# Kernel optimization log

Measured on AMD Instinct MI355X. Metric: run time of the kernel, lower is better.

## Reference

```python
import jax, jax.numpy as jnp
import numpy as np

B, C, H, W = 32, 256, 32, 32
C8 = C // 8


def setup_inputs() -> dict:
    key = jax.random.key(0)
    ks = jax.random.split(key, 8)
    s = 1.0 / np.sqrt(C)
    return {
        "x": jax.random.normal(ks[0], (B, C, H, W), dtype=jnp.float32),
        "Wq": jax.random.normal(ks[1], (C8, C), dtype=jnp.float32) * s,
        "bq": jax.random.normal(ks[2], (C8,), dtype=jnp.float32) * s,
        "Wk": jax.random.normal(ks[3], (C8, C), dtype=jnp.float32) * s,
        "bk": jax.random.normal(ks[4], (C8,), dtype=jnp.float32) * s,
        "Wv": jax.random.normal(ks[5], (C, C), dtype=jnp.float32) * s,
        "bv": jax.random.normal(ks[6], (C,), dtype=jnp.float32) * s,
        "gamma": jax.random.normal(ks[7], (1,), dtype=jnp.float32) * 0.1,
    }


def reference(x, Wq, bq, Wk, bk, Wv, bv, gamma):
    b, c, h, w = x.shape
    n = h * w
    xf = x.reshape(b, c, n)  # [B, C, N]
    # 1x1 convs == per-pixel linear projections
    q = jnp.einsum('dc,bcn->bnd', Wq, xf) + bq            # [B, N, C/8]
    k = jnp.einsum('dc,bcn->bdn', Wk, xf) + bk[:, None]    # [B, C/8, N]
    v = jnp.einsum('dc,bcn->bdn', Wv, xf) + bv[:, None]    # [B, C, N]
    energy = jnp.einsum('bnd,bdm->bnm', q, k)              # [B, N, N], no scaling (as in source)
    attn = jax.nn.softmax(energy, axis=-1)                 # softmax over keys
    # out[:, :, i] = sum_j V[:, :, j] * attn[i, j]
    out = jnp.einsum('bdn,bmn->bdm', v, attn)              # [B, C, N]
    out = out.reshape(b, c, h, w)
    return gamma * out + x
```

## Files before the change

### kernel.cpp

```cpp
#include <hip/hip_runtime.h>
#include <math.h>

#define BB 32
#define CC 256
#define CQ 32
#define NN 1024

typedef short bf16x8 __attribute__((ext_vector_type(8)));
typedef float f32x4  __attribute__((ext_vector_type(4)));
typedef unsigned short u16;

__device__ __forceinline__ u16 f2bf(float f) {
    unsigned u = __float_as_uint(f);
    u = (u + 0x7FFFu + ((u >> 16) & 1u)) >> 16;
    return (u16)u;
}

__device__ __forceinline__ unsigned cvt_pk_bf16(float lo, float hi) {
    unsigned r;
    asm("v_cvt_pk_bf16_f32 %0, %1, %2" : "=v"(r) : "v"(lo), "v"(hi));
    return r;
}

__global__ void wpack_kernel(const float* __restrict__ Wq,
                             const float* __restrict__ Wk,
                             const float* __restrict__ Wv,
                             u16* __restrict__ wfrag)
{
    const int o = blockIdx.x * 256 + threadIdx.x;
    const int j    = o & 7;
    const int lane = (o >> 3) & 63;
    const int kc   = (o >> 9) & 7;
    const int rt   = o >> 12;
    const int row  = rt * 16 + (lane & 15);
    const int col  = kc * 32 + (lane >> 4) * 8 + j;
    const float v = (row < 32) ? Wq[row * 256 + col]
                  : (row < 64) ? Wk[(row - 32) * 256 + col]
                               : Wv[(row - 64) * 256 + col];
    wfrag[o] = f2bf(v);
}

struct QSmem {
    union {
        u16 xs[64][268];
        u16 osv[CC][72];
    };
    u16 osqk[64][72];
};

__global__ __launch_bounds__(256, 2) void qkv_kernel(
    const float* __restrict__ x, const u16* __restrict__ wfrag,
    const float* __restrict__ bq, const float* __restrict__ bk,
    const float* __restrict__ bv,
    u16* __restrict__ qt, u16* __restrict__ kt, u16* __restrict__ vv)
{
    __shared__ QSmem sm;
    const int b = blockIdx.y, n0 = blockIdx.x * 64;
    const int t = threadIdx.x;
    const int lane = t & 63, w = t >> 6;
    const int quad = lane >> 4, c16 = lane & 15;

    {
        const float* xb = x + (size_t)b * CC * NN + n0;
        const int n2 = 2 * (lane & 31);
        const int cr = w * 2 + (lane >> 5);
        float2 f[32];
#pragma unroll
        for (int it = 0; it < 32; ++it)
            f[it] = *(const float2*)(xb + (size_t)(it * 8 + cr) * NN + n2);
#pragma unroll
        for (int it = 0; it < 32; ++it) {
            const int c = it * 8 + cr;
            sm.xs[n2 + 0][c] = f2bf(f[it].x);
            sm.xs[n2 + 1][c] = f2bf(f[it].y);
        }
    }
    __syncthreads();

    f32x4 acc[5][4];
#pragma unroll
    for (int i = 0; i < 5; ++i)
#pragma unroll
        for (int j = 0; j < 4; ++j) acc[i][j] = (f32x4){0.f, 0.f, 0.f, 0.f};

#pragma unroll 2
    for (int k = 0; k < 8; ++k) {
        const int c0 = k * 32;
        bf16x8 wa[5], xb[4];
#pragma unroll
        for (int rs = 0; rs < 5; ++rs)
            wa[rs] = *(const bf16x8*)&wfrag[(size_t)(((w * 5 + rs) * 8 + k) * 64 + lane) * 8];
#pragma unroll
        for (int ns = 0; ns < 4; ++ns) {
            const short4 a = *(const short4*)&sm.xs[ns * 16 + c16][c0 + quad * 8];
            const short4 b2 = *(const short4*)&sm.xs[ns * 16 + c16][c0 + quad * 8 + 4];
            bf16x8 v;
            v[0] = a.x; v[1] = a.y; v[2] = a.z; v[3] = a.w;
            v[4] = b2.x; v[5] = b2.y; v[6] = b2.z; v[7] = b2.w;
            xb[ns] = v;
        }
#pragma unroll
        for (int rs = 0; rs < 5; ++rs)
#pragma unroll
            for (int ns = 0; ns < 4; ++ns)
                acc[rs][ns] = __builtin_amdgcn_mfma_f32_16x16x32_bf16(
                    wa[rs], xb[ns], acc[rs][ns], 0, 0, 0);
    }

    __syncthreads();

#pragma unroll
    for (int rs = 0; rs < 5; ++rs) {
#pragma unroll
        for (int r = 0; r < 4; ++r) {
            const int rg = w * 80 + rs * 16 + quad * 4 + r;
            const float bias = (rg < 32) ? bq[rg] : (rg < 64) ? bk[rg - 32] : bv[rg - 64];
#pragma unroll
            for (int ns = 0; ns < 4; ++ns) {
                const int n = ns * 16 + c16;
                const u16 h = f2bf(acc[rs][ns][r] + bias);
                if (rg < 64) sm.osqk[n][rg] = h;
                else         sm.osv[rg - 64][n] = h;
            }
        }
    }
    __syncthreads();

    {
        u16* dst = (w >= 2) ? kt : qt;
        const int dof = (w >= 2) ? 32 : 0;
        const int wl = w & 1;
        const size_t base = ((size_t)b * NN + n0) * CQ;
#pragma unroll
        for (int it = 0; it < 4; ++it) {
            const int o = wl * 2048 + it * 512 + lane * 8;
            const int n = o >> 5, d = o & 31;
            const bf16x8 v = *(const bf16x8*)&sm.osqk[n][d + dof];
            *(bf16x8*)&dst[base + o] = v;
        }
    }
#pragma unroll
    for (int it = 0; it < 8; ++it) {
        const int o = it * 2048 + t * 8;
        const int c = o >> 6, n = o & 63;
        const bf16x8 v = *(const bf16x8*)&sm.osv[c][n];
        *(bf16x8*)&vv[((size_t)b * CC + c) * NN + n0 + n] = v;
    }
}

__global__ __launch_bounds__(512, 4) void attn_kernel(
    const u16* __restrict__ qt, const u16* __restrict__ kt,
    const u16* __restrict__ vv, const float* __restrict__ x,
    const float* __restrict__ gamma_p, float* __restrict__ out)
{
    __shared__ u16 ps16[2][64][72];
    __shared__ float lsh[64];

    const int bid  = blockIdx.x;
    const int xcd  = bid & 7;
    const int slot = bid >> 3;
    const int b    = (xcd << 2) | (slot >> 4);
    const int m0   = (slot & 15) * 64;

    const int t = threadIdx.x, lane = t & 63, w = t >> 6;
    const int quad = lane >> 4, c16 = lane & 15;
    const int ch   = c16 >> 3;
    const int c7   = c16 & 7;
    const int qkey = (c16 >> 2) & 3;
    const int sm   = w & 3;
    const int sh   = w >> 2;
    const int ms0  = w & 3;

    const bf16x8 qa = *(const bf16x8*)&qt[((size_t)b * NN + m0 + sm * 16 + c16) * CQ + quad * 8];

    bf16x8 ones;
#pragma unroll
    for (int j = 0; j < 8; ++j) ones[j] = (short)0x3F80;

    f32x4 accO[2][4];
    f32x4 lsum = (f32x4){0.f, 0.f, 0.f, 0.f};
#pragma unroll
    for (int cs = 0; cs < 2; ++cs)
#pragma unroll
        for (int j = 0; j < 4; ++j) accO[cs][j] = (f32x4){0.f, 0.f, 0.f, 0.f};

    const u16* vbase = vv + (size_t)b * CC * NN;
    const u16* kbase = kt + (size_t)b * NN * CQ;

    bf16x8 kb[2];
#pragma unroll
    for (int s = 0; s < 2; ++s)
        kb[s] = *(const bf16x8*)&kbase[(size_t)(sh * 32 + s * 16 + c16) * CQ + quad * 8];

    for (int step = 0; step < 16; ++step) {
        const int nbase = step * 64;
        u16* psb = &ps16[step & 1][0][0];

        bf16x8 va[2][2];
#pragma unroll
        for (int cs = 0; cs < 2; ++cs)
#pragma unroll
            for (int kc = 0; kc < 2; ++kc)
                va[cs][kc] = *(const bf16x8*)&vbase[
                    (size_t)(w * 32 + cs * 16 + c16) * NN + nbase + kc * 32 + quad * 8];

        f32x4 accS[2];
#pragma unroll
        for (int s = 0; s < 2; ++s)
            accS[s] = __builtin_amdgcn_mfma_f32_16x16x32_bf16(
                qa, kb[s], (f32x4){0.f, 0.f, 0.f, 0.f}, 0, 0, 0);

        const int rowb = sm * 16 + quad * 4;
#pragma unroll
        for (int s = 0; s < 2; ++s) {
            const int nb = (sh * 4 + 2 * s + ch) ^ quad;
            u16* pw = &psb[rowb * 72 + nb * 8 + c7];
            const float e0 = __expf(accS[s][0]);
            const float e1 = __expf(accS[s][1]);
            const float e2 = __expf(accS[s][2]);
            const float e3 = __expf(accS[s][3]);
            const unsigned p01 = cvt_pk_bf16(e0, e1);
            const unsigned p23 = cvt_pk_bf16(e2, e3);
            pw[0]       = (u16)p01;
            pw[72]      = (u16)(p01 >> 16);
            pw[144]     = (u16)p23;
            pw[216]     = (u16)(p23 >> 16);
        }

        if (step < 15) {
#pragma unroll
            for (int s = 0; s < 2; ++s)
                kb[s] = *(const bf16x8*)&kbase[
                    (size_t)(nbase + 64 + sh * 32 + s * 16 + c16) * CQ + quad * 8];
        }

        __syncthreads();

#pragma unroll
        for (int msi = 0; msi < 4; ++msi) {
            bf16x8 pb[2];
#pragma unroll
            for (int kc = 0; kc < 2; ++kc)
                pb[kc] = *(const bf16x8*)&psb[(msi * 16 + c16) * 72
                                              + (4 * kc + (quad ^ qkey)) * 8];
            if (msi == ms0) {
                lsum = __builtin_amdgcn_mfma_f32_16x16x32_bf16(ones, pb[0], lsum, 0, 0, 0);
                lsum = __builtin_amdgcn_mfma_f32_16x16x32_bf16(ones, pb[1], lsum, 0, 0, 0);
            }
#pragma unroll
            for (int cs = 0; cs < 2; ++cs)
#pragma unroll
                for (int kc = 0; kc < 2; ++kc)
                    accO[cs][msi] = __builtin_amdgcn_mfma_f32_16x16x32_bf16(
                        va[cs][kc], pb[kc], accO[cs][msi], 0, 0, 0);
        }
    }

    if (sh == 0 && quad == 0) lsh[ms0 * 16 + c16] = lsum[0];
    __syncthreads();

    const float gamma = gamma_p[0];
#pragma unroll
    for (int ms = 0; ms < 4; ++ms) {
        const float inv = gamma / lsh[ms * 16 + c16];
        const int m = m0 + ms * 16 + c16;
#pragma unroll
        for (int cs = 0; cs < 2; ++cs) {
            const int cbase = w * 32 + cs * 16 + quad * 4;
#pragma unroll
            for (int r = 0; r < 4; ++r) {
                const size_t idx = ((size_t)b * CC + cbase + r) * NN + m;
                out[idx] = accO[cs][ms][r] * inv + x[idx];
            }
        }
    }
}

extern "C" void kernel_launch(void* const* d_in, const int* in_sizes, int n_in,
                              void* d_out, int out_size, void* d_ws, size_t ws_size,
                              hipStream_t stream)
{
    const float* x  = (const float*)d_in[0];
    const float* Wq = (const float*)d_in[1];
    const float* bq = (const float*)d_in[2];
    const float* Wk = (const float*)d_in[3];
    const float* bk = (const float*)d_in[4];
    const float* Wv = (const float*)d_in[5];
    const float* bv = (const float*)d_in[6];
    const float* gm = (const float*)d_in[7];
    float* out = (float*)d_out;

    u16* qt    = (u16*)d_ws;
    u16* kt    = qt + (size_t)BB * NN * CQ;
    u16* vv    = kt + (size_t)BB * NN * CQ;
    u16* wfrag = vv + (size_t)BB * CC * NN;

    wpack_kernel<<<320, 256, 0, stream>>>(Wq, Wk, Wv, wfrag);
    dim3 grid(16, BB);
    qkv_kernel<<<grid, 256, 0, stream>>>(x, wfrag, bq, bk, bv, qt, kt, vv);
    attn_kernel<<<512, 512, 0, stream>>>(qt, kt, vv, x, gm, out);
}
```

Baseline: 152.9 us.

## Halve QKV pixel tile and double attention key-step width with priority hints

```diff
diff --git a/kernel.cpp b/kernel.cpp
--- a/kernel.cpp
+++ b/kernel.cpp
@@ -42,56 +42,58 @@
 
 struct QSmem {
     union {
-        u16 xs[64][268];
-        u16 osv[CC][72];
+        u16 xs[32][268];
+        u16 osv[CC][40];
     };
-    u16 osqk[64][72];
+    u16 osqk[32][72];
 };
 
-__global__ __launch_bounds__(256, 2) void qkv_kernel(
+__global__ __launch_bounds__(256, 4) void qkv_kernel(
     const float* __restrict__ x, const u16* __restrict__ wfrag,
     const float* __restrict__ bq, const float* __restrict__ bk,
     const float* __restrict__ bv,
     u16* __restrict__ qt, u16* __restrict__ kt, u16* __restrict__ vv)
 {
     __shared__ QSmem sm;
-    const int b = blockIdx.y, n0 = blockIdx.x * 64;
+    const int b = blockIdx.y, n0 = blockIdx.x * 32;
     const int t = threadIdx.x;
     const int lane = t & 63, w = t >> 6;
     const int quad = lane >> 4, c16 = lane & 15;
 
     {
         const float* xb = x + (size_t)b * CC * NN + n0;
-        const int n2 = 2 * (lane & 31);
-        const int cr = w * 2 + (lane >> 5);
-        float2 f[32];
-#pragma unroll
-        for (int it = 0; it < 32; ++it)
-            f[it] = *(const float2*)(xb + (size_t)(it * 8 + cr) * NN + n2);
-#pragma unroll
-        for (int it = 0; it < 32; ++it) {
-            const int c = it * 8 + cr;
-            sm.xs[n2 + 0][c] = f2bf(f[it].x);
-            sm.xs[n2 + 1][c] = f2bf(f[it].y);
+        const int n4 = (t & 7) * 4;
+        const int cr = t >> 3;
+        float4 f[8];
+#pragma unroll
+        for (int it = 0; it < 8; ++it)
+            f[it] = *(const float4*)(xb + (size_t)(it * 32 + cr) * NN + n4);
+#pragma unroll
+        for (int it = 0; it < 8; ++it) {
+            const int c = it * 32 + cr;
+            sm.xs[n4 + 0][c] = f2bf(f[it].x);
+            sm.xs[n4 + 1][c] = f2bf(f[it].y);
+            sm.xs[n4 + 2][c] = f2bf(f[it].z);
+            sm.xs[n4 + 3][c] = f2bf(f[it].w);
         }
     }
     __syncthreads();
 
-    f32x4 acc[5][4];
+    f32x4 acc[5][2];
 #pragma unroll
     for (int i = 0; i < 5; ++i)
 #pragma unroll
-        for (int j = 0; j < 4; ++j) acc[i][j] = (f32x4){0.f, 0.f, 0.f, 0.f};
+        for (int j = 0; j < 2; ++j) acc[i][j] = (f32x4){0.f, 0.f, 0.f, 0.f};
 
 #pragma unroll 2
     for (int k = 0; k < 8; ++k) {
         const int c0 = k * 32;
-        bf16x8 wa[5], xb[4];
+        bf16x8 wa[5], xb[2];
 #pragma unroll
         for (int rs = 0; rs < 5; ++rs)
             wa[rs] = *(const bf16x8*)&wfrag[(size_t)(((w * 5 + rs) * 8 + k) * 64 + lane) * 8];
 #pragma unroll
-        for (int ns = 0; ns < 4; ++ns) {
+        for (int ns = 0; ns < 2; ++ns) {
             const short4 a = *(const short4*)&sm.xs[ns * 16 + c16][c0 + quad * 8];
             const short4 b2 = *(const short4*)&sm.xs[ns * 16 + c16][c0 + quad * 8 + 4];
             bf16x8 v;
@@ -102,7 +104,7 @@
 #pragma unroll
         for (int rs = 0; rs < 5; ++rs)
 #pragma unroll
-            for (int ns = 0; ns < 4; ++ns)
+            for (int ns = 0; ns < 2; ++ns)
                 acc[rs][ns] = __builtin_amdgcn_mfma_f32_16x16x32_bf16(
                     wa[rs], xb[ns], acc[rs][ns], 0, 0, 0);
     }
@@ -116,7 +118,7 @@
             const int rg = w * 80 + rs * 16 + quad * 4 + r;
             const float bias = (rg < 32) ? bq[rg] : (rg < 64) ? bk[rg - 32] : bv[rg - 64];
 #pragma unroll
-            for (int ns = 0; ns < 4; ++ns) {
+            for (int ns = 0; ns < 2; ++ns) {
                 const int n = ns * 16 + c16;
                 const u16 h = f2bf(acc[rs][ns][r] + bias);
                 if (rg < 64) sm.osqk[n][rg] = h;
@@ -127,22 +129,17 @@
     __syncthreads();
 
     {
-        u16* dst = (w >= 2) ? kt : qt;
-        const int dof = (w >= 2) ? 32 : 0;
-        const int wl = w & 1;
-        const size_t base = ((size_t)b * NN + n0) * CQ;
-#pragma unroll
-        for (int it = 0; it < 4; ++it) {
-            const int o = wl * 2048 + it * 512 + lane * 8;
-            const int n = o >> 5, d = o & 31;
-            const bf16x8 v = *(const bf16x8*)&sm.osqk[n][d + dof];
-            *(bf16x8*)&dst[base + o] = v;
-        }
-    }
-#pragma unroll
-    for (int it = 0; it < 8; ++it) {
+        u16* dst = (t >= 128) ? kt : qt;
+        const int dof = (t >= 128) ? 32 : 0;
+        const int o = (t & 127) * 8;
+        const int n = o >> 5, d = o & 31;
+        const bf16x8 v = *(const bf16x8*)&sm.osqk[n][d + dof];
+        *(bf16x8*)&dst[((size_t)b * NN + n0) * CQ + o] = v;
+    }
+#pragma unroll
+    for (int it = 0; it < 4; ++it) {
         const int o = it * 2048 + t * 8;
-        const int c = o >> 6, n = o & 63;
+        const int c = o >> 5, n = o & 31;
         const bf16x8 v = *(const bf16x8*)&sm.osv[c][n];
         *(bf16x8*)&vv[((size_t)b * CC + c) * NN + n0 + n] = v;
     }
@@ -153,7 +150,7 @@
     const u16* __restrict__ vv, const float* __restrict__ x,
     const float* __restrict__ gamma_p, float* __restrict__ out)
 {
-    __shared__ u16 ps16[2][64][72];
+    __shared__ u16 ps16[2][64][136];
     __shared__ float lsh[64];
 
     const int bid  = blockIdx.x;
@@ -187,73 +184,79 @@
     const u16* vbase = vv + (size_t)b * CC * NN;
     const u16* kbase = kt + (size_t)b * NN * CQ;
 
-    bf16x8 kb[2];
-#pragma unroll
-    for (int s = 0; s < 2; ++s)
-        kb[s] = *(const bf16x8*)&kbase[(size_t)(sh * 32 + s * 16 + c16) * CQ + quad * 8];
-
-    for (int step = 0; step < 16; ++step) {
-        const int nbase = step * 64;
+    bf16x8 kb[4];
+#pragma unroll
+    for (int s = 0; s < 4; ++s)
+        kb[s] = *(const bf16x8*)&kbase[(size_t)(sh * 64 + s * 16 + c16) * CQ + quad * 8];
+
+    for (int step = 0; step < 8; ++step) {
+        const int nbase = step * 128;
         u16* psb = &ps16[step & 1][0][0];
 
-        bf16x8 va[2][2];
+        bf16x8 va[2][4];
 #pragma unroll
         for (int cs = 0; cs < 2; ++cs)
 #pragma unroll
-            for (int kc = 0; kc < 2; ++kc)
+            for (int kc = 0; kc < 4; ++kc)
                 va[cs][kc] = *(const bf16x8*)&vbase[
                     (size_t)(w * 32 + cs * 16 + c16) * NN + nbase + kc * 32 + quad * 8];
 
-        f32x4 accS[2];
-#pragma unroll
-        for (int s = 0; s < 2; ++s)
+        f32x4 accS[4];
+#pragma unroll
+        for (int s = 0; s < 4; ++s)
             accS[s] = __builtin_amdgcn_mfma_f32_16x16x32_bf16(
                 qa, kb[s], (f32x4){0.f, 0.f, 0.f, 0.f}, 0, 0, 0);
 
         const int rowb = sm * 16 + quad * 4;
 #pragma unroll
-        for (int s = 0; s < 2; ++s) {
-            const int nb = (sh * 4 + 2 * s + ch) ^ quad;
-            u16* pw = &psb[rowb * 72 + nb * 8 + c7];
+        for (int s = 0; s < 4; ++s) {
+            const int nbt = sh * 8 + 2 * s + ch;
+            const int p = nbt ^ quad;
+            u16* pw = &psb[rowb * 136 + p * 8 + c7];
             const float e0 = __expf(accS[s][0]);
             const float e1 = __expf(accS[s][1]);
             const float e2 = __expf(accS[s][2]);
             const float e3 = __expf(accS[s][3]);
             const unsigned p01 = cvt_pk_bf16(e0, e1);
             const unsigned p23 = cvt_pk_bf16(e2, e3);
-            pw[0]       = (u16)p01;
-            pw[72]      = (u16)(p01 >> 16);
-            pw[144]     = (u16)p23;
-            pw[216]     = (u16)(p23 >> 16);
-        }
-
-        if (step < 15) {
-#pragma unroll
-            for (int s = 0; s < 2; ++s)
+            pw[0]   = (u16)p01;
+            pw[136] = (u16)(p01 >> 16);
+            pw[272] = (u16)p23;
+            pw[408] = (u16)(p23 >> 16);
+        }
+
+        if (step < 7) {
+#pragma unroll
+            for (int s = 0; s < 4; ++s)
                 kb[s] = *(const bf16x8*)&kbase[
-                    (size_t)(nbase + 64 + sh * 32 + s * 16 + c16) * CQ + quad * 8];
-        }
-
-        __syncthreads();
-
+                    (size_t)(nbase + 128 + sh * 64 + s * 16 + c16) * CQ + quad * 8];
+        }
+
+        asm volatile("s_waitcnt lgkmcnt(0)" ::: "memory");
+        __builtin_amdgcn_s_barrier();
+        asm volatile("" ::: "memory");
+
+        __builtin_amdgcn_s_setprio(1);
 #pragma unroll
         for (int msi = 0; msi < 4; ++msi) {
-            bf16x8 pb[2];
-#pragma unroll
-            for (int kc = 0; kc < 2; ++kc)
-                pb[kc] = *(const bf16x8*)&psb[(msi * 16 + c16) * 72
+            bf16x8 pb[4];
+#pragma unroll
+            for (int kc = 0; kc < 4; ++kc)
+                pb[kc] = *(const bf16x8*)&psb[(msi * 16 + c16) * 136
                                               + (4 * kc + (quad ^ qkey)) * 8];
             if (msi == ms0) {
-                lsum = __builtin_amdgcn_mfma_f32_16x16x32_bf16(ones, pb[0], lsum, 0, 0, 0);
-                lsum = __builtin_amdgcn_mfma_f32_16x16x32_bf16(ones, pb[1], lsum, 0, 0, 0);
+#pragma unroll
+                for (int kc = 0; kc < 4; ++kc)
+                    lsum = __builtin_amdgcn_mfma_f32_16x16x32_bf16(ones, pb[kc], lsum, 0, 0, 0);
             }
 #pragma unroll
             for (int cs = 0; cs < 2; ++cs)
 #pragma unroll
-                for (int kc = 0; kc < 2; ++kc)
+                for (int kc = 0; kc < 4; ++kc)
                     accO[cs][msi] = __builtin_amdgcn_mfma_f32_16x16x32_bf16(
                         va[cs][kc], pb[kc], accO[cs][msi], 0, 0, 0);
         }
+        __builtin_amdgcn_s_setprio(0);
     }
 
     if (sh == 0 && quad == 0) lsh[ms0 * 16 + c16] = lsum[0];
@@ -296,7 +299,7 @@
     u16* wfrag = vv + (size_t)BB * CC * NN;
 
     wpack_kernel<<<320, 256, 0, stream>>>(Wq, Wk, Wv, wfrag);
-    dim3 grid(16, BB);
+    dim3 grid(32, BB);
     qkv_kernel<<<grid, 256, 0, stream>>>(x, wfrag, bq, bk, bv, qt, kt, vv);
     attn_kernel<<<512, 512, 0, stream>>>(qt, kt, vv, x, gm, out);
 }
```

Result: no change. 150.9 us (-1.3%).
